# Kernel optimization log

Hardware: AMD Instinct MI355X
Metric: run time of the kernel (lower is better)

## Reference

```python
import jax, jax.numpy as jnp
import numpy as np

IN_F, OUT_F = 4096, 14336
F8_MAX = 448.0  # max magnitude of float8_e4m3fn


def setup_inputs() -> dict:
    key = jax.random.key(0)
    kx, kw, kb = jax.random.split(key, 3)
    x = jax.random.normal(kx, (2, 512, IN_F), dtype=jnp.bfloat16)
    w = jax.random.normal(kw, (OUT_F, IN_F), dtype=jnp.float32) * 0.02
    # per-tensor scale: amax / 448 (as in F8Linear.__init__)
    w_scale = (jnp.maximum(jnp.abs(w).max(), 1e-30) / F8_MAX).astype(jnp.float32)
    # quantize to fp8 e4m3; roundtrip back to float32 so the stored values are
    # exactly the fp8-representable values (float32 container keeps the bwd
    # reference's jax.vjp happy while the math is identical)
    w_f8 = jnp.clip(w / w_scale, -F8_MAX, F8_MAX).astype(jnp.float8_e4m3fn).astype(jnp.float32)
    bias = jax.random.normal(kb, (OUT_F,), dtype=jnp.float32) * 0.02
    return {"x": x, "weight_f8": w_f8, "w_scale": w_scale, "bias": bias}


def reference(x, weight_f8, w_scale, bias):
    # dequantize to activation dtype, then GEMM: y = x @ w^T + b
    w = weight_f8.astype(x.dtype) * w_scale.astype(x.dtype)   # [out, in]
    y = jnp.einsum('bsi,oi->bso', x, w) + bias.astype(x.dtype)
    return y
```

## Files before the change

kernel.cpp:

```cpp
#include <hip/hip_runtime.h>
#include <hip/hip_bf16.h>
#include <stdint.h>


#define IN_F   4096
#define OUT_F  14336
#define M_TOT  1024

#define BM 128
#define BN 128

#define TM 256
#define TN 256
#define TK 64
#define KT8 (IN_F / TK)

typedef __bf16  bf16x8 __attribute__((ext_vector_type(8)));
typedef __bf16  bf16x4 __attribute__((ext_vector_type(4)));
typedef float   f32x4  __attribute__((ext_vector_type(4)));

__device__ __forceinline__ void async_copy16(const void* g, void* l) {
    __builtin_amdgcn_global_load_lds(
        (const __attribute__((address_space(1))) void*)g,
        (__attribute__((address_space(3))) void*)l,
        16, 0, 0);
}

__global__ void detect_x_dtype(const uint32_t* __restrict__ xb,
                               int* __restrict__ flag) {
    __shared__ int any_low;
    if (threadIdx.x == 0) any_low = 0;
    __syncthreads();
    uint32_t bad = 0;
    for (int i = threadIdx.x; i < 1024; i += 256) bad |= (xb[i] & 0xFFFFu);
    if (bad) atomicOr(&any_low, 1);
    __syncthreads();
    if (threadIdx.x == 0) *flag = (any_low == 0) ? 1 : 0;
}

__global__ __launch_bounds__(256) void cvt_x_kernel(
    const void* __restrict__ xraw, bf16x8* __restrict__ out,
    const int* __restrict__ flag) {
    const int f32w = (*flag != 0);
    const int i = blockIdx.x * 256 + threadIdx.x;
    if (f32w) {
        const f32x4* in = (const f32x4*)xraw;
        f32x4 a = in[2 * i];
        f32x4 b = in[2 * i + 1];
        bf16x8 o;
        o[0] = (__bf16)a[0]; o[1] = (__bf16)a[1];
        o[2] = (__bf16)a[2]; o[3] = (__bf16)a[3];
        o[4] = (__bf16)b[0]; o[5] = (__bf16)b[1];
        o[6] = (__bf16)b[2]; o[7] = (__bf16)b[3];
        out[i] = o;
    } else {
        out[i] = ((const bf16x8*)xraw)[i];
    }
}

__global__ __launch_bounds__(512, 2) void gemm_fused_8ph(
    const __bf16* __restrict__ xb,
    const float*  __restrict__ wf,
    const float*  __restrict__ w_scale,
    const float*  __restrict__ bias,
    void*         __restrict__ yraw,
    const int*    __restrict__ flag_p)
{
    __shared__ __align__(16) __bf16 As[2][2][128 * TK];
    __shared__ __align__(16) __bf16 Bs[2][2][128 * TK];

    const int f32w = (*flag_p != 0);
    const int t    = threadIdx.x;
    const int lane = t & 63;
    const int wv   = t >> 6;
    const int wm   = wv >> 2;
    const int wn   = wv & 3;
    const int lidx = lane & 15;
    const int q    = lane >> 4;

    const int flat = blockIdx.x;
    const int xcd  = flat & 7;
    const int slot = flat >> 3;
    const int ni   = xcd * 7 + (slot >> 2);
    const int mi   = slot & 3;
    const int m0   = mi * TM;
    const int n0   = ni * TN;

    const float scale = w_scale[0];

    const __bf16* gA = xb + (size_t)m0 * IN_F;

    int srow[2], scgl[2];
    #pragma unroll
    for (int i = 0; i < 2; ++i) {
        const int s = i * 512 + t;
        srow[i] = s >> 3;
        scgl[i] = (s & 7) ^ (srow[i] & 7);
    }

    const float* gB0 = wf + (size_t)(n0 + srow[0]) * IN_F + scgl[0] * 8;
    const float* gB1 = wf + (size_t)(n0 + srow[1]) * IN_F + scgl[1] * 8;

    int aoff[4][2], boff[2][2];
    #pragma unroll
    for (int qm = 0; qm < 4; ++qm) {
        const int row = qm * 32 + wm * 16 + lidx;
        #pragma unroll
        for (int kg = 0; kg < 2; ++kg)
            aoff[qm][kg] = row * 128 + (((kg * 4 + q) ^ (row & 7)) * 16);
    }
    #pragma unroll
    for (int qn = 0; qn < 2; ++qn) {
        const int row = qn * 64 + wn * 16 + lidx;
        #pragma unroll
        for (int kg = 0; kg < 2; ++kg)
            boff[qn][kg] = row * 128 + (((kg * 4 + q) ^ (row & 7)) * 16);
    }

    const f32x4 zero4 = {0.f, 0.f, 0.f, 0.f};
    f32x4 acc[8][4];
    #pragma unroll
    for (int i = 0; i < 8; ++i)
        #pragma unroll
        for (int j = 0; j < 4; ++j)
            acc[i][j] = zero4;

    bf16x8 areg[4][2], breg[2][2];
    f32x4 Br0[4], Br1[4];

#define STAGE_A(tile, half, BI) do {                                          \
    __bf16* _dst = &As[(BI)][(half)][0];                                      \
    const __bf16* _src = gA + (size_t)(half) * 128 * IN_F + (tile) * TK;      \
    async_copy16(_src + (size_t)srow[0] * IN_F + scgl[0] * 8, _dst + t * 8);  \
    async_copy16(_src + (size_t)srow[1] * IN_F + scgl[1] * 8,                 \
                 _dst + (512 + t) * 8);                                       \
} while (0)

#define B_LOAD(tile, half, Rv) do {                                           \
    const float* _p0 = gB0 + (size_t)(half) * 128 * IN_F + (tile) * TK;       \
    const float* _p1 = gB1 + (size_t)(half) * 128 * IN_F + (tile) * TK;       \
    Rv[0] = *(const f32x4*)_p0;                                               \
    Rv[1] = *(const f32x4*)(_p0 + 4);                                         \
    Rv[2] = *(const f32x4*)_p1;                                               \
    Rv[3] = *(const f32x4*)(_p1 + 4);                                         \
} while (0)

#define B_WRITE(half, BI, Rv) do {                                            \
    __bf16* _d = &Bs[(BI)][(half)][0];                                        \
    bf16x8 _o;                                                                \
    _o[0] = (__bf16)Rv[0][0]; _o[1] = (__bf16)Rv[0][1];                       \
    _o[2] = (__bf16)Rv[0][2]; _o[3] = (__bf16)Rv[0][3];                       \
    _o[4] = (__bf16)Rv[1][0]; _o[5] = (__bf16)Rv[1][1];                       \
    _o[6] = (__bf16)Rv[1][2]; _o[7] = (__bf16)Rv[1][3];                       \
    *(bf16x8*)(_d + (size_t)t * 8) = _o;                                      \
    _o[0] = (__bf16)Rv[2][0]; _o[1] = (__bf16)Rv[2][1];                       \
    _o[2] = (__bf16)Rv[2][2]; _o[3] = (__bf16)Rv[2][3];                       \
    _o[4] = (__bf16)Rv[3][0]; _o[5] = (__bf16)Rv[3][1];                       \
    _o[6] = (__bf16)Rv[3][2]; _o[7] = (__bf16)Rv[3][3];                       \
    *(bf16x8*)(_d + (size_t)(512 + t) * 8) = _o;                              \
} while (0)

#define LOAD_A(base) do {                                                     \
    _Pragma("unroll")                                                         \
    for (int _qm = 0; _qm < 4; ++_qm) {                                       \
        areg[_qm][0] = *(const bf16x8*)((base) + aoff[_qm][0]);               \
        areg[_qm][1] = *(const bf16x8*)((base) + aoff[_qm][1]);               \
    }                                                                         \
} while (0)

#define LOAD_B(base) do {                                                     \
    _Pragma("unroll")                                                         \
    for (int _qn = 0; _qn < 2; ++_qn) {                                       \
        breg[_qn][0] = *(const bf16x8*)((base) + boff[_qn][0]);               \
        breg[_qn][1] = *(const bf16x8*)((base) + boff[_qn][1]);               \
    }                                                                         \
} while (0)

#define MFMA16(MO, NO) do {                                                   \
    __builtin_amdgcn_s_setprio(1);                                            \
    _Pragma("unroll")                                                         \
    for (int _qm = 0; _qm < 4; ++_qm)                                         \
        _Pragma("unroll")                                                     \
        for (int _qn = 0; _qn < 2; ++_qn) {                                   \
            acc[(MO) + _qm][(NO) + _qn] =                                     \
                __builtin_amdgcn_mfma_f32_16x16x32_bf16(                      \
                    areg[_qm][0], breg[_qn][0], acc[(MO) + _qm][(NO) + _qn],  \
                    0, 0, 0);                                                 \
            acc[(MO) + _qm][(NO) + _qn] =                                     \
                __builtin_amdgcn_mfma_f32_16x16x32_bf16(                      \
                    areg[_qm][1], breg[_qn][1], acc[(MO) + _qm][(NO) + _qn],  \
                    0, 0, 0);                                                 \
        }                                                                     \
    __builtin_amdgcn_s_setprio(0);                                            \
} while (0)

#define BARR()    __builtin_amdgcn_s_barrier()
#define LGKM0()   asm volatile("s_waitcnt lgkmcnt(0)" ::: "memory")
#define VMCNT(n)  asm volatile("s_waitcnt vmcnt(" #n ")" ::: "memory")

    B_LOAD(0, 0, Br0);
    B_LOAD(0, 1, Br1);
    STAGE_A(0, 0, 0);
    STAGE_A(0, 1, 0);
    VMCNT(4);
    B_WRITE(0, 0, Br0);
    B_WRITE(1, 0, Br1);
    STAGE_A(1, 0, 1);
    VMCNT(2);
    LGKM0();
    BARR();

#define TILE_BODY(kt, P, QI) do {                                             \
    const char* _a0 = (const char*)&As[(P)][0][0];                            \
    const char* _a1 = (const char*)&As[(P)][1][0];                            \
    const char* _b0 = (const char*)&Bs[(P)][0][0];                            \
    const char* _b1 = (const char*)&Bs[(P)][1][0];                            \
                \
    LOAD_A(_a0);                                                              \
    LOAD_B(_b0);                                                              \
    if ((kt) + 1 < KT8) { B_LOAD((kt) + 1, 0, Br0);                           \
                          B_LOAD((kt) + 1, 1, Br1); }                         \
    BARR(); LGKM0();                                                          \
    MFMA16(0, 0);                                                             \
    BARR();                                                                   \
                                \
    LOAD_B(_b1);                                                              \
    if ((kt) + 1 < KT8) STAGE_A((kt) + 1, 1, QI);                             \
    BARR(); LGKM0();                                                          \
    MFMA16(0, 2);                                                             \
    BARR();                                                                   \
         \
         \
    LOAD_A(_a1);                                                              \
    if ((kt) + 2 < KT8) STAGE_A((kt) + 2, 0, P);                              \
    BARR(); LGKM0();                                                          \
    MFMA16(4, 2);                                                             \
    BARR();                                                                   \
         \
         \
         \
         \
    LOAD_B(_b0);                                                              \
    BARR(); LGKM0();                                                          \
    MFMA16(4, 0);                                                             \
    if ((kt) < KT8 - 2)      { VMCNT(2); }                                    \
    else                     { VMCNT(0); }                                    \
    if ((kt) + 1 < KT8) {                                                     \
        B_WRITE(0, QI, Br0);                                                  \
        B_WRITE(1, QI, Br1);                                                  \
        LGKM0();                                                              \
    }                                                                         \
    BARR();                                                                   \
} while (0)

    for (int it = 0; it < KT8 / 2; ++it) {
        const int kte = 2 * it;
        TILE_BODY(kte,     0, 1);
        TILE_BODY(kte + 1, 1, 0);
    }

#undef TILE_BODY
#undef STAGE_A
#undef B_LOAD
#undef B_WRITE
#undef LOAD_A
#undef LOAD_B
#undef MFMA16
#undef BARR
#undef LGKM0
#undef VMCNT

    float bv[4];
    #pragma unroll
    for (int nf = 0; nf < 4; ++nf)
        bv[nf] = bias[n0 + (nf >> 1) * 128 + (nf & 1) * 64 + wn * 16 + lidx];

    if (f32w) {
        float* yf = (float*)yraw;
        #pragma unroll
        for (int mf = 0; mf < 8; ++mf)
            #pragma unroll
            for (int r = 0; r < 4; ++r) {
                const int m = m0 + (mf >> 2) * 128 + (mf & 3) * 32 + wm * 16 + q * 4 + r;
                float* yp = yf + (size_t)m * OUT_F + n0 + wn * 16 + lidx;
                #pragma unroll
                for (int nf = 0; nf < 4; ++nf)
                    yp[(nf >> 1) * 128 + (nf & 1) * 64] =
                        acc[mf][nf][r] * scale + bv[nf];
            }
    } else {
        __bf16* yh = (__bf16*)yraw;
        #pragma unroll
        for (int mf = 0; mf < 8; ++mf)
            #pragma unroll
            for (int r = 0; r < 4; ++r) {
                const int m = m0 + (mf >> 2) * 128 + (mf & 3) * 32 + wm * 16 + q * 4 + r;
                __bf16* yp = yh + (size_t)m * OUT_F + n0 + wn * 16 + lidx;
                #pragma unroll
                for (int nf = 0; nf < 4; ++nf)
                    yp[(nf >> 1) * 128 + (nf & 1) * 64] =
                        (__bf16)(acc[mf][nf][r] * scale + bv[nf]);
            }
    }
}

__global__ __launch_bounds__(256) void f8linear_fallback(
    const void*  __restrict__ xraw,
    const float* __restrict__ wq,
    const float* __restrict__ w_scale,
    const float* __restrict__ bias,
    void*        __restrict__ yraw,
    const int*   __restrict__ flag_p)
{
    __shared__ __align__(16) __bf16 As[BM * 40];
    __shared__ __align__(16) __bf16 Bs[BN * 40];

    const int f32w = (*flag_p != 0);
    const int t    = threadIdx.x;
    const int lane = t & 63;
    const int wv   = t >> 6;
    const int wm   = wv >> 1;
    const int wn   = wv & 1;
    const int lidx = lane & 15;
    const int q    = lane >> 4;

    const int flat = blockIdx.x;
    const int xcd  = flat & 7;
    const int slot = flat >> 3;
    const int ni   = xcd * 14 + (slot >> 3);
    const int mi   = slot & 7;
    const int m0   = mi * BM;
    const int n0   = ni * BN;

    const float scale = w_scale[0];
    const float*  xf = (const float*)xraw;
    const __bf16* xh = (const __bf16*)xraw;

    const int af_row = t >> 3;
    const int af_col = (t & 7) * 4;
    int ah_row[2], ah_cg[2];
    #pragma unroll
    for (int i = 0; i < 2; ++i) {
        const int s = i * 256 + t;
        ah_row[i] = s >> 2;
        ah_cg[i]  = s & 3;
    }
    const int b_row = t >> 3;
    const int b_col = (t & 7) * 4;

    const f32x4 zero4 = {0.f, 0.f, 0.f, 0.f};
    f32x4 acc[4][4];
    #pragma unroll
    for (int i = 0; i < 4; ++i)
        #pragma unroll
        for (int j = 0; j < 4; ++j)
            acc[i][j] = zero4;

    f32x4  aregf[4];
    bf16x8 aregh[2];
    f32x4  breg[4];
    if (f32w) {
        #pragma unroll
        for (int i = 0; i < 4; ++i)
            aregf[i] = *reinterpret_cast<const f32x4*>(
                xf + (size_t)(m0 + af_row + i * 32) * IN_F + af_col);
    } else {
        #pragma unroll
        for (int i = 0; i < 2; ++i)
            aregh[i] = *reinterpret_cast<const bf16x8*>(
                xh + (size_t)(m0 + ah_row[i]) * IN_F + ah_cg[i] * 8);
    }
    #pragma unroll
    for (int i = 0; i < 4; ++i)
        breg[i] = *reinterpret_cast<const f32x4*>(
            wq + (size_t)(n0 + i * 32 + b_row) * IN_F + b_col);

    for (int kt = 0; kt < 128; ++kt) {
        const int k0 = kt * 32;
        if (f32w) {
            #pragma unroll
            for (int i = 0; i < 4; ++i) {
                bf16x4 pk;
                pk[0] = (__bf16)aregf[i][0];
                pk[1] = (__bf16)aregf[i][1];
                pk[2] = (__bf16)aregf[i][2];
                pk[3] = (__bf16)aregf[i][3];
                *reinterpret_cast<bf16x4*>(As + (af_row + i * 32) * 40 + af_col) = pk;
            }
        } else {
            #pragma unroll
            for (int i = 0; i < 2; ++i)
                *reinterpret_cast<bf16x8*>(As + ah_row[i] * 40 + ah_cg[i] * 8) = aregh[i];
        }
        #pragma unroll
        for (int i = 0; i < 4; ++i) {
            bf16x4 pk;
            pk[0] = (__bf16)breg[i][0];
            pk[1] = (__bf16)breg[i][1];
            pk[2] = (__bf16)breg[i][2];
            pk[3] = (__bf16)breg[i][3];
            *reinterpret_cast<bf16x4*>(Bs + (i * 32 + b_row) * 40 + b_col) = pk;
        }
        __syncthreads();
        if (kt + 1 < 128) {
            const int k1 = k0 + 32;
            if (f32w) {
                #pragma unroll
                for (int i = 0; i < 4; ++i)
                    aregf[i] = *reinterpret_cast<const f32x4*>(
                        xf + (size_t)(m0 + af_row + i * 32) * IN_F + k1 + af_col);
            } else {
                #pragma unroll
                for (int i = 0; i < 2; ++i)
                    aregh[i] = *reinterpret_cast<const bf16x8*>(
                        xh + (size_t)(m0 + ah_row[i]) * IN_F + k1 + ah_cg[i] * 8);
            }
            #pragma unroll
            for (int i = 0; i < 4; ++i)
                breg[i] = *reinterpret_cast<const f32x4*>(
                    wq + (size_t)(n0 + i * 32 + b_row) * IN_F + k1 + b_col);
        }
        bf16x8 afr[4], bfr[4];
        #pragma unroll
        for (int mt = 0; mt < 4; ++mt) {
            const int row = wm * 64 + mt * 16 + lidx;
            afr[mt] = *reinterpret_cast<const bf16x8*>(As + row * 40 + q * 8);
        }
        #pragma unroll
        for (int nt = 0; nt < 4; ++nt) {
            const int row = wn * 64 + nt * 16 + lidx;
            bfr[nt] = *reinterpret_cast<const bf16x8*>(Bs + row * 40 + q * 8);
        }
        #pragma unroll
        for (int mt = 0; mt < 4; ++mt)
            #pragma unroll
            for (int nt = 0; nt < 4; ++nt)
                acc[mt][nt] = __builtin_amdgcn_mfma_f32_16x16x32_bf16(
                    afr[mt], bfr[nt], acc[mt][nt], 0, 0, 0);
        __syncthreads();
    }

    float bv[4];
    #pragma unroll
    for (int nt = 0; nt < 4; ++nt)
        bv[nt] = bias[n0 + wn * 64 + nt * 16 + lidx];

    if (f32w) {
        float* yf = (float*)yraw;
        #pragma unroll
        for (int mt = 0; mt < 4; ++mt)
            #pragma unroll
            for (int r = 0; r < 4; ++r) {
                const int m = m0 + wm * 64 + mt * 16 + q * 4 + r;
                float* yp = yf + (size_t)m * OUT_F + n0 + wn * 64 + lidx;
                #pragma unroll
                for (int nt = 0; nt < 4; ++nt)
                    yp[nt * 16] = acc[mt][nt][r] * scale + bv[nt];
            }
    } else {
        __bf16* yh = (__bf16*)yraw;
        #pragma unroll
        for (int mt = 0; mt < 4; ++mt)
            #pragma unroll
            for (int r = 0; r < 4; ++r) {
                const int m = m0 + wm * 64 + mt * 16 + q * 4 + r;
                __bf16* yp = yh + (size_t)m * OUT_F + n0 + wn * 64 + lidx;
                #pragma unroll
                for (int nt = 0; nt < 4; ++nt)
                    yp[nt * 16] = (__bf16)(acc[mt][nt][r] * scale + bv[nt]);
            }
    }
}

extern "C" void kernel_launch(void* const* d_in, const int* in_sizes, int n_in,
                              void* d_out, int out_size, void* d_ws, size_t ws_size,
                              hipStream_t stream) {
    const void* px = nullptr; const void* pw = nullptr;
    const void* ps = nullptr; const void* pb = nullptr;
    for (int i = 0; i < n_in; ++i) {
        const long sz = in_sizes[i];
        if      (sz == (long)M_TOT * IN_F) px = d_in[i];
        else if (sz == (long)OUT_F * IN_F) pw = d_in[i];
        else if (sz == 1)                  ps = d_in[i];
        else if (sz == OUT_F)              pb = d_in[i];
    }
    if (!px) px = d_in[0];
    if (!pw) pw = d_in[1];
    if (!ps) ps = d_in[2];
    if (!pb) pb = d_in[3];

    const size_t X_BYTES  = (size_t)M_TOT * IN_F * 2;
    const size_t FLAG_OFF = X_BYTES;

    if (ws_size >= FLAG_OFF + 16) {
        __bf16* xbf  = (__bf16*)d_ws;
        int*    flag = (int*)((char*)d_ws + FLAG_OFF);

        const int grid8 = (M_TOT / TM) * (OUT_F / TN);

        detect_x_dtype<<<1, 256, 0, stream>>>((const uint32_t*)px, flag);
        cvt_x_kernel<<<2048, 256, 0, stream>>>(px, (bf16x8*)xbf, flag);
        gemm_fused_8ph<<<grid8, 512, 0, stream>>>(
            xbf, (const float*)pw, (const float*)ps, (const float*)pb,
            d_out, flag);
    } else {
        int* flag = (int*)d_ws;
        const int grid = (M_TOT / BM) * (OUT_F / BN);
        detect_x_dtype<<<1, 256, 0, stream>>>((const uint32_t*)px, flag);
        f8linear_fallback<<<grid, 256, 0, stream>>>(
            px, (const float*)pw, (const float*)ps, (const float*)pb, d_out, flag);
    }
}
```

Baseline: 467.8 us.

## Replace eight-phase barrier schedule with single-barrier-per-tile pipeline

Rewrites the main K loop so that all global loads for the next tile (B register loads and A LDS staging) are issued at the top of each tile. The four MFMA phases then run back to back with no intermediate barriers, followed by a single vmcnt(0)/lgkmcnt(0) wait and one barrier per tile. The s_setprio hints around the MFMA groups are also removed. This cuts barrier count and wait overhead, but the fine-grained interleaving of memory and compute across waves is lost, and waiting on vmcnt(0) every tile may expose global-load latency.

```diff
diff --git a/kernel.cpp b/kernel.cpp
--- a/kernel.cpp
+++ b/kernel.cpp
@@ -58,7 +58,7 @@
     }
 }
 
-__global__ __launch_bounds__(512, 2) void gemm_fused_8ph(
+__global__ __launch_bounds__(512, 2) void gemm_fused_1b(
     const __bf16* __restrict__ xb,
     const float*  __restrict__ wf,
     const float*  __restrict__ w_scale,
@@ -177,7 +177,6 @@
 } while (0)
 
 #define MFMA16(MO, NO) do {                                                   \
-    __builtin_amdgcn_s_setprio(1);                                            \
     _Pragma("unroll")                                                         \
     for (int _qm = 0; _qm < 4; ++_qm)                                         \
         _Pragma("unroll")                                                     \
@@ -191,22 +190,20 @@
                     areg[_qm][1], breg[_qn][1], acc[(MO) + _qm][(NO) + _qn],  \
                     0, 0, 0);                                                 \
         }                                                                     \
-    __builtin_amdgcn_s_setprio(0);                                            \
-} while (0)
-
-#define BARR()    __builtin_amdgcn_s_barrier()
+} while (0)
+
+#define BARR()    do { __builtin_amdgcn_s_barrier();                          \
+                       asm volatile("" ::: "memory"); } while (0)
 #define LGKM0()   asm volatile("s_waitcnt lgkmcnt(0)" ::: "memory")
-#define VMCNT(n)  asm volatile("s_waitcnt vmcnt(" #n ")" ::: "memory")
+#define VMCNT0()  asm volatile("s_waitcnt vmcnt(0)" ::: "memory")
 
     B_LOAD(0, 0, Br0);
     B_LOAD(0, 1, Br1);
     STAGE_A(0, 0, 0);
     STAGE_A(0, 1, 0);
-    VMCNT(4);
+    VMCNT0();
     B_WRITE(0, 0, Br0);
     B_WRITE(1, 0, Br1);
-    STAGE_A(1, 0, 1);
-    VMCNT(2);
     LGKM0();
     BARR();
 
@@ -215,41 +212,27 @@
     const char* _a1 = (const char*)&As[(P)][1][0];                            \
     const char* _b0 = (const char*)&Bs[(P)][0][0];                            \
     const char* _b1 = (const char*)&Bs[(P)][1][0];                            \
-                \
+    if ((kt) + 1 < KT8) {                                                     \
+        B_LOAD((kt) + 1, 0, Br0);                                             \
+        B_LOAD((kt) + 1, 1, Br1);                                             \
+        STAGE_A((kt) + 1, 0, QI);                                             \
+        STAGE_A((kt) + 1, 1, QI);                                             \
+    }                                                                         \
     LOAD_A(_a0);                                                              \
     LOAD_B(_b0);                                                              \
-    if ((kt) + 1 < KT8) { B_LOAD((kt) + 1, 0, Br0);                           \
-                          B_LOAD((kt) + 1, 1, Br1); }                         \
-    BARR(); LGKM0();                                                          \
     MFMA16(0, 0);                                                             \
-    BARR();                                                                   \
-                                \
     LOAD_B(_b1);                                                              \
-    if ((kt) + 1 < KT8) STAGE_A((kt) + 1, 1, QI);                             \
-    BARR(); LGKM0();                                                          \
     MFMA16(0, 2);                                                             \
-    BARR();                                                                   \
-         \
-         \
     LOAD_A(_a1);                                                              \
-    if ((kt) + 2 < KT8) STAGE_A((kt) + 2, 0, P);                              \
-    BARR(); LGKM0();                                                          \
     MFMA16(4, 2);                                                             \
-    BARR();                                                                   \
-         \
-         \
-         \
-         \
     LOAD_B(_b0);                                                              \
-    BARR(); LGKM0();                                                          \
     MFMA16(4, 0);                                                             \
-    if ((kt) < KT8 - 2)      { VMCNT(2); }                                    \
-    else                     { VMCNT(0); }                                    \
+    VMCNT0();      \
     if ((kt) + 1 < KT8) {                                                     \
         B_WRITE(0, QI, Br0);                                                  \
         B_WRITE(1, QI, Br1);                                                  \
-        LGKM0();                                                              \
     }                                                                         \
+    LGKM0();                   \
     BARR();                                                                   \
 } while (0)
 
@@ -268,7 +251,7 @@
 #undef MFMA16
 #undef BARR
 #undef LGKM0
-#undef VMCNT
+#undef VMCNT0
 
     float bv[4];
     #pragma unroll
@@ -500,7 +483,7 @@
 
         detect_x_dtype<<<1, 256, 0, stream>>>((const uint32_t*)px, flag);
         cvt_x_kernel<<<2048, 256, 0, stream>>>(px, (bf16x8*)xbf, flag);
-        gemm_fused_8ph<<<grid8, 512, 0, stream>>>(
+        gemm_fused_1b<<<grid8, 512, 0, stream>>>(
             xbf, (const float*)pw, (const float*)ps, (const float*)pb,
             d_out, flag);
     } else {
```

Result: no change. 465.0 us (-0.6%).
